# Optimization experiments

Measured on AMD Instinct MI355X. Metric: run time of the kernel, lower is better.

The kernel has to match this reference:

```python
import jax, jax.numpy as jnp
import numpy as np

B, L, DM, DIN, N, R, K, H = 4, 2048, 1024, 2048, 16, 64, 4, 1024
EPS = 1e-5


def setup_inputs() -> dict:
    key = jax.random.key(0)
    ks = jax.random.split(key, 12)
    nrm = lambda k, shp, s=0.02: jax.random.normal(k, shp, jnp.float32) * s
    return dict(
        hidden_states=jax.random.normal(ks[0], (B, L, DM), jnp.float32),
        residual=jax.random.normal(ks[1], (B, L, DM), jnp.float32),
        norm_w=jnp.ones((DM,), jnp.float32),
        in_proj_w=nrm(ks[2], (2 * DIN, DM)),
        conv_w=nrm(ks[3], (DIN, K), 0.2),
        conv_b=jnp.zeros((DIN,), jnp.float32),
        x_proj_w=nrm(ks[4], (R + 2 * N, DIN)),
        dt_proj_w=nrm(ks[5], (DIN, R), 0.1),
        dt_proj_b=jnp.log(jnp.expm1(jnp.full((DIN,), 0.01, jnp.float32))),
        A_log=jnp.log(jnp.tile(jnp.arange(1, N + 1, dtype=jnp.float32), (DIN, 1))),
        D=jnp.ones((DIN,), jnp.float32),
        out_proj_w=nrm(ks[6], (DM, DIN)),
        norm2_w=jnp.ones((DM,), jnp.float32),
        fc1_w=nrm(ks[7], (2 * H, DM)),
        fc2_w=nrm(ks[8], (DM, H)),
    )


def _rmsnorm(x, w):
    return x * jax.lax.rsqrt(jnp.mean(x * x, axis=-1, keepdims=True) + EPS) * w


def _mixer(h, in_proj_w, conv_w, conv_b, x_proj_w, dt_proj_w, dt_proj_b,
           A_log, D, out_proj_w):
    # in_proj -> x, z : (B, L, DIN) each
    xz = jnp.einsum('bld,ed->ble', h, in_proj_w)
    x, z = jnp.split(xz, 2, axis=-1)
    # depthwise causal conv along L
    xc = x.transpose(0, 2, 1)  # (B, DIN, L)
    xc = jax.lax.conv_general_dilated(
        xc, conv_w[:, None, :], window_strides=(1,), padding=[(K - 1, 0)],
        feature_group_count=DIN)
    xc = xc + conv_b[None, :, None]
    x = jax.nn.silu(xc).transpose(0, 2, 1)  # (B, L, DIN)
    # x_proj -> dt_low, B, C
    dbl = jnp.einsum('bld,ed->ble', x, x_proj_w)
    dt_low, Bm, Cm = jnp.split(dbl, [R, R + N], axis=-1)
    dt = jax.nn.softplus(jnp.einsum('blr,dr->bld', dt_low, dt_proj_w) + dt_proj_b)
    A = -jnp.exp(A_log)  # (DIN, N)

    def step(hc, inp):
        dt_t, B_t, C_t, x_t = inp  # (B,DIN),(B,N),(B,N),(B,DIN)
        hc = jnp.exp(dt_t[..., None] * A) * hc + (dt_t * x_t)[..., None] * B_t[:, None, :]
        return hc, jnp.einsum('bdn,bn->bd', hc, C_t)

    h0 = jnp.zeros((B, DIN, N), x.dtype)
    _, ys = jax.lax.scan(step, h0, (dt.transpose(1, 0, 2), Bm.transpose(1, 0, 2),
                                    Cm.transpose(1, 0, 2), x.transpose(1, 0, 2)))
    y = ys.transpose(1, 0, 2) + x * D  # skip term D*u
    y = y * jax.nn.silu(z)
    return jnp.einsum('bld,ed->ble', y, out_proj_w)


def reference(hidden_states, residual, norm_w, in_proj_w, conv_w, conv_b,
              x_proj_w, dt_proj_w, dt_proj_b, A_log, D, out_proj_w,
              norm2_w, fc1_w, fc2_w):
    # pre-norm residual path (fused_add_norm=False, residual_in_fp32=True)
    res = hidden_states + residual
    hn = _rmsnorm(res, norm_w)
    mix = _mixer(hn, in_proj_w, conv_w, conv_b, x_proj_w, dt_proj_w,
                 dt_proj_b, A_log, D, out_proj_w)
    # NOTE: faithful to source: residual is overwritten by norm2(mix+res),
    # while mlp is applied to the raw mixer output.
    res2 = _rmsnorm(mix + res, norm2_w)
    fc = jnp.einsum('bld,hd->blh', mix, fc1_w)
    y, gate = jnp.split(fc, 2, axis=-1)
    out = jnp.einsum('blh,dh->bld', y * jax.nn.silu(gate), fc2_w)
    return (out, res2)
```

## Files before the change

kernel.cpp:

```cpp
#include <hip/hip_runtime.h>
#include <hip/hip_bf16.h>

#define B_   4
#define L_   2048
#define DM_  1024
#define DIN_ 2048
#define NS_  16
#define R_   64
#define KC_  4
#define H_   1024
#define BL_  (B_ * L_)

typedef __attribute__((ext_vector_type(4))) float f32x4;
typedef __attribute__((ext_vector_type(8))) short bf16x8;
typedef __attribute__((ext_vector_type(8))) unsigned short u16x8;

#if __has_builtin(__builtin_amdgcn_exp2f)
#define EXP2(x) __builtin_amdgcn_exp2f(x)
#else
#define EXP2(x) exp2f(x)
#endif
#define LOG2E 1.44269504088896f

__device__ __forceinline__ float b2f(unsigned short u) {
    union { unsigned int i; float f; } v; v.i = ((unsigned int)u) << 16; return v.f;
}
__device__ __forceinline__ unsigned short f2b(float f) {
    union { float f; unsigned int i; } v; v.f = f;
    unsigned int r = v.i + 0x7fffu + ((v.i >> 16) & 1u);
    return (unsigned short)(r >> 16);
}
__device__ __forceinline__ float sigmoidf_(float x) { return 1.f / (1.f + __expf(-x)); }
__device__ __forceinline__ float softplusf_(float x) { return (x > 20.f) ? x : log1pf(__expf(x)); }

__device__ __forceinline__ void gload16(const unsigned short* g, unsigned short* l) {
    __builtin_amdgcn_global_load_lds(
        (__attribute__((address_space(1))) void*)(g),
        (__attribute__((address_space(3))) void*)(l), 16, 0, 0);
}

__global__ void k_cvt4(const float* __restrict__ in, unsigned short* __restrict__ out, int n4) {
    int i = blockIdx.x * blockDim.x + threadIdx.x;
    if (i < n4) {
        float4 v = ((const float4*)in)[i];
        ((ushort4*)out)[i] = make_ushort4(f2b(v.x), f2b(v.y), f2b(v.z), f2b(v.w));
    }
}
__global__ void k_fill04(unsigned short* __restrict__ out, int n4) {
    int i = blockIdx.x * blockDim.x + threadIdx.x;
    if (i < n4) ((ushort4*)out)[i] = make_ushort4(0, 0, 0, 0);
}

__global__ __launch_bounds__(256)
void k_reduceX(const float* __restrict__ part, unsigned short* __restrict__ dblB,
               float* __restrict__ dblF) {
    int i = blockIdx.x * 256 + threadIdx.x;
    if (i >= BL_ * 96) return;
    int r = i / 96, n = i - r * 96;
    const float* p = part + (size_t)r * 2048;
    float s = p[n] + p[128 + n] + p[256 + n] + p[384 + n];
    dblB[(size_t)r * 96 + n] = f2b(s);
    if (n >= 64) dblF[(size_t)r * 32 + n - 64] = s;
}

__global__ __launch_bounds__(256)
void k_add_rmsnorm(const float* __restrict__ a, const float* __restrict__ b,
                   const float* __restrict__ w,
                   float* __restrict__ resOut, unsigned short* __restrict__ hnOut) {
    int row = blockIdx.x, tid = threadIdx.x;
    const float4* ap = (const float4*)(a + (size_t)row * DM_);
    const float4* bp = (const float4*)(b + (size_t)row * DM_);
    float4 va = ap[tid], vb = bp[tid];
    float4 s = make_float4(va.x + vb.x, va.y + vb.y, va.z + vb.z, va.w + vb.w);
    ((float4*)(resOut + (size_t)row * DM_))[tid] = s;
    float ss = s.x * s.x + s.y * s.y + s.z * s.z + s.w * s.w;
    #pragma unroll
    for (int m = 32; m >= 1; m >>= 1) ss += __shfl_xor(ss, m);
    __shared__ float red[4];
    if ((tid & 63) == 0) red[tid >> 6] = ss;
    __syncthreads();
    float tot = red[0] + red[1] + red[2] + red[3];
    float sc = rsqrtf(tot / (float)DM_ + 1e-5f);
    float4 vw = ((const float4*)w)[tid];
    unsigned short* hp = hnOut + (size_t)row * DM_ + tid * 4;
    *(ushort4*)hp = make_ushort4(f2b(s.x * sc * vw.x), f2b(s.y * sc * vw.y),
                                 f2b(s.z * sc * vw.z), f2b(s.w * sc * vw.w));
}

__global__ __launch_bounds__(256)
void k_add_rmsnorm2(const float* __restrict__ mix, const float* __restrict__ res,
                    const float* __restrict__ w,
                    float* __restrict__ res2Out, unsigned short* __restrict__ mixB) {
    int row = blockIdx.x, tid = threadIdx.x;
    const float4* mp = (const float4*)(mix + (size_t)row * DM_);
    const float4* rp = (const float4*)(res + (size_t)row * DM_);
    float4 vm = mp[tid], vr = rp[tid];
    float4 s = make_float4(vm.x + vr.x, vm.y + vr.y, vm.z + vr.z, vm.w + vr.w);
    unsigned short* mb = mixB + (size_t)row * DM_ + tid * 4;
    *(ushort4*)mb = make_ushort4(f2b(vm.x), f2b(vm.y), f2b(vm.z), f2b(vm.w));
    float ss = s.x * s.x + s.y * s.y + s.z * s.z + s.w * s.w;
    #pragma unroll
    for (int m = 32; m >= 1; m >>= 1) ss += __shfl_xor(ss, m);
    __shared__ float red[4];
    if ((tid & 63) == 0) red[tid >> 6] = ss;
    __syncthreads();
    float tot = red[0] + red[1] + red[2] + red[3];
    float sc = rsqrtf(tot / (float)DM_ + 1e-5f);
    float4 vw = ((const float4*)w)[tid];
    float4 o = make_float4(s.x * sc * vw.x, s.y * sc * vw.y, s.z * sc * vw.z, s.w * sc * vw.w);
    ((float4*)(res2Out + (size_t)row * DM_))[tid] = o;
}

__global__ __launch_bounds__(256)
void k_conv_silu(const unsigned short* __restrict__ xz,
                 const float* __restrict__ cw, const float* __restrict__ cb,
                 unsigned short* __restrict__ xc) {
    const int tid = threadIdx.x;
    const int d0 = tid * 8;
    const int b  = blockIdx.x >> 8;
    const int t0 = (blockIdx.x & 255) * 8;
    const unsigned short* xbase = xz + (size_t)b * L_ * (2 * DIN_) + d0;
    unsigned short* obase = xc + (size_t)b * L_ * DIN_ + d0;

    float4 w[8];
    float bias[8];
    #pragma unroll
    for (int j = 0; j < 8; j++) {
        w[j] = ((const float4*)cw)[d0 + j];
        bias[j] = cb[d0 + j];
    }
    u16x8 zero = (u16x8){0, 0, 0, 0, 0, 0, 0, 0};
    u16x8 r0 = zero, r1 = zero, r2 = zero, r3;
    if (t0 >= 3) {
        r0 = *(const u16x8*)(xbase + (size_t)(t0 - 3) * (2 * DIN_));
        r1 = *(const u16x8*)(xbase + (size_t)(t0 - 2) * (2 * DIN_));
        r2 = *(const u16x8*)(xbase + (size_t)(t0 - 1) * (2 * DIN_));
    }
    #pragma unroll
    for (int tt = 0; tt < 8; tt++) {
        int t = t0 + tt;
        r3 = *(const u16x8*)(xbase + (size_t)t * (2 * DIN_));
        u16x8 out;
        #pragma unroll
        for (int j = 0; j < 8; j++) {
            float acc = bias[j] + w[j].x * b2f(r0[j]) + w[j].y * b2f(r1[j])
                                + w[j].z * b2f(r2[j]) + w[j].w * b2f(r3[j]);
            out[j] = f2b(acc * sigmoidf_(acc));
        }
        *(u16x8*)(obase + (size_t)t * DIN_) = out;
        r0 = r1; r1 = r2; r2 = r3;
    }
}

__global__ __launch_bounds__(256)
void k_gate(const unsigned short* __restrict__ fc, unsigned short* __restrict__ g) {
    int i = blockIdx.x * 256 + threadIdx.x;
    int row = i >> 7;
    int h8 = (i & 127) * 8;
    u16x8 y8 = *(const u16x8*)(fc + (size_t)row * (2 * H_) + h8);
    u16x8 g8 = *(const u16x8*)(fc + (size_t)row * (2 * H_) + H_ + h8);
    u16x8 o;
    #pragma unroll
    for (int j = 0; j < 8; j++) {
        float y = b2f(y8[j]), gt = b2f(g8[j]);
        o[j] = f2b(y * gt * sigmoidf_(gt));
    }
    *(u16x8*)(g + (size_t)row * H_ + h8) = o;
}

template <int CHLT>
__global__ __launch_bounds__(256)
void k_scan_p1(const unsigned short* __restrict__ dty, const unsigned short* __restrict__ xc,
               const float* __restrict__ dblF, const float* __restrict__ A_log,
               unsigned short* __restrict__ Q, unsigned short* __restrict__ sumdt, int cch) {
    const int tid = threadIdx.x;
    const int d = (blockIdx.x & 7) * 256 + tid;
    const int b = blockIdx.x >> 3;
    const int c = blockIdx.y;
    const int t0 = c * CHLT;

    float a[NS_], h[NS_];
    #pragma unroll
    for (int n = 0; n < NS_; n++) { a[n] = -__expf(A_log[d * NS_ + n]) * LOG2E; h[n] = 0.f; }
    float sd = 0.f;

    const unsigned short* dp  = dty + (size_t)b * L_ * DIN_ + d;
    const unsigned short* xp  = xc  + (size_t)b * L_ * DIN_ + d;
    const float* bcp = dblF + (size_t)(b * L_ + t0) * 32;

    #pragma unroll 2
    for (int t = 0; t < CHLT; t++) {
        int tg = t0 + t;
        float dtv = b2f(dp[(size_t)tg * DIN_]);
        float xv  = b2f(xp[(size_t)tg * DIN_]);
        sd += dtv;
        float bx = dtv * xv;
        const float* bc = bcp + t * 32;
        #pragma unroll
        for (int n = 0; n < NS_; n++)
            h[n] = EXP2(dtv * a[n]) * h[n] + bx * bc[n];
    }
    unsigned short* q = Q + ((size_t)(b * cch + c) * DIN_ + d) * NS_;
    u16x8 qa, qb;
    #pragma unroll
    for (int j = 0; j < 8; j++) { qa[j] = f2b(h[j]); qb[j] = f2b(h[8 + j]); }
    *(u16x8*)q = qa;
    *(u16x8*)(q + 8) = qb;
    sumdt[(size_t)(b * cch + c) * DIN_ + d] = f2b(sd);
}

__global__ __launch_bounds__(256)
void k_scan_comb(unsigned short* __restrict__ Q, const unsigned short* __restrict__ sumdt,
                 const float* __restrict__ A_log, int cch) {
    int i = blockIdx.x * 256 + threadIdx.x;
    int n = i & 15;
    int d = (i >> 4) & (DIN_ - 1);
    int b = i >> 15;
    float a = -__expf(A_log[d * NS_ + n]) * LOG2E;
    float h = 0.f;
    for (int c = 0; c < cch; c++) {
        size_t base = ((size_t)(b * cch + c) * DIN_ + d);
        float q  = b2f(Q[base * NS_ + n]);
        float sd = b2f(sumdt[base]);
        if (c > 0) Q[((size_t)(b * cch + c - 1) * DIN_ + d) * NS_ + n] = f2b(h);
        h = EXP2(a * sd) * h + q;
    }
}

template <int CHLT>
__global__ __launch_bounds__(256)
void k_scan_p3(unsigned short* __restrict__ dty, const unsigned short* __restrict__ xc,
               const float* __restrict__ dblF, const float* __restrict__ A_log,
               const float* __restrict__ Dp, const unsigned short* __restrict__ xz,
               const unsigned short* __restrict__ Qh, int cch) {
    const int tid = threadIdx.x;
    const int d = (blockIdx.x & 7) * 256 + tid;
    const int b = blockIdx.x >> 3;
    const int c = blockIdx.y;
    const int t0 = c * CHLT;

    float a[NS_], h[NS_];
    #pragma unroll
    for (int n = 0; n < NS_; n++) a[n] = -__expf(A_log[d * NS_ + n]) * LOG2E;
    if (c == 0) {
        #pragma unroll
        for (int n = 0; n < NS_; n++) h[n] = 0.f;
    } else {
        const unsigned short* qh = Qh + ((size_t)(b * cch + c - 1) * DIN_ + d) * NS_;
        u16x8 v0 = *(const u16x8*)qh;
        u16x8 v1 = *(const u16x8*)(qh + 8);
        #pragma unroll
        for (int j = 0; j < 8; j++) { h[j] = b2f(v0[j]); h[8 + j] = b2f(v1[j]); }
    }
    float Dd = Dp[d];

    unsigned short* dp = dty + (size_t)b * L_ * DIN_ + d;
    const unsigned short* xp  = xc + (size_t)b * L_ * DIN_ + d;
    const unsigned short* zp  = xz + (size_t)b * L_ * (2 * DIN_) + DIN_ + d;
    const float* bcp = dblF + (size_t)(b * L_ + t0) * 32;

    #pragma unroll 2
    for (int t = 0; t < CHLT; t++) {
        int tg = t0 + t;
        float dtv = b2f(dp[(size_t)tg * DIN_]);
        float xv  = b2f(xp[(size_t)tg * DIN_]);
        float bx = dtv * xv;
        const float* bc = bcp + t * 32;
        float y = 0.f;
        #pragma unroll
        for (int n = 0; n < NS_; n++) {
            h[n] = EXP2(dtv * a[n]) * h[n] + bx * bc[n];
            y += h[n] * bc[16 + n];
        }
        y += xv * Dd;
        float zv = b2f(zp[(size_t)tg * (2 * DIN_)]);
        dp[(size_t)tg * DIN_] = f2b(y * zv * sigmoidf_(zv));
    }
}

template <int EPI, int SPLITK = 0>
__global__ __launch_bounds__(256)
void k_gemm(const unsigned short* __restrict__ A, int lda,
            const unsigned short* __restrict__ Bw, int ldb,
            void* __restrict__ outp, int ldc, const float* __restrict__ bias,
            int M, int N, int Kd, int Nstore) {
    if constexpr (SPLITK) {
        const int z = blockIdx.z;
        A += (size_t)z * 512;
        Bw += (size_t)z * 512;
        outp = (void*)((float*)outp + z * 128);
    }
    __shared__ unsigned short As[128 * 32];
    __shared__ unsigned short Bs[128 * 32];
    const int tid = threadIdx.x;
    const int lane = tid & 63;
    const int w = tid >> 6;
    const int wr = w >> 1, wc = w & 1;
    const int bm = blockIdx.y * 128, bn = blockIdx.x * 128;

    const int e0 = tid * 8;
    const int r0 = e0 >> 5;
    const int c0 = e0 & 31;
    const int r1 = r0 + 64;

    f32x4 acc[4][4];
    #pragma unroll
    for (int i = 0; i < 4; i++)
        #pragma unroll
        for (int j = 0; j < 4; j++) acc[i][j] = (f32x4){0.f, 0.f, 0.f, 0.f};

    const int fr = lane & 15, ko = (lane >> 4) * 8;

    for (int k0 = 0; k0 < Kd; k0 += 32) {
        gload16(A  + (size_t)(bm + r0) * lda + k0 + c0, &As[e0]);
        gload16(A  + (size_t)(bm + r1) * lda + k0 + c0, &As[e0 + 2048]);
        gload16(Bw + (size_t)(bn + r0) * ldb + k0 + c0, &Bs[e0]);
        gload16(Bw + (size_t)(bn + r1) * ldb + k0 + c0, &Bs[e0 + 2048]);
        __syncthreads();
        bf16x8 af[4], bv[4];
        #pragma unroll
        for (int i = 0; i < 4; i++)
            af[i] = *(const bf16x8*)&As[(wr * 64 + i * 16 + fr) * 32 + ko];
        #pragma unroll
        for (int j = 0; j < 4; j++)
            bv[j] = *(const bf16x8*)&Bs[(wc * 64 + j * 16 + fr) * 32 + ko];
        #pragma unroll
        for (int i = 0; i < 4; i++)
            #pragma unroll
            for (int j = 0; j < 4; j++)
                acc[i][j] = __builtin_amdgcn_mfma_f32_16x16x32_bf16(af[i], bv[j], acc[i][j], 0, 0, 0);
        __syncthreads();
    }

    const int rr = (lane >> 4) * 4;
    const int cc = lane & 15;
    #pragma unroll
    for (int i = 0; i < 4; i++) {
        #pragma unroll
        for (int j = 0; j < 4; j++) {
            int col = bn + wc * 64 + j * 16 + cc;
            if (col >= Nstore) continue;
            #pragma unroll
            for (int q = 0; q < 4; q++) {
                int row = bm + wr * 64 + i * 16 + rr + q;
                float v = acc[i][j][q];
                if constexpr (EPI == 2) { v += bias[col]; v = softplusf_(v); }
                if constexpr (EPI == 0)
                    ((float*)outp)[(size_t)row * ldc + col] = v;
                else
                    ((unsigned short*)outp)[(size_t)row * ldc + col] = f2b(v);
            }
        }
    }
}

#define SBAR   __builtin_amdgcn_s_barrier()
#define SCHED0 __builtin_amdgcn_sched_barrier(0)
#define SLOT(r) ((((r) ^ ((r) >> 2)) & 3) << 4)

template <int EPI, int BN>
__global__ __launch_bounds__(512, 2)
void k_gemm256(const unsigned short* __restrict__ Aptr, int lda,
               const unsigned short* __restrict__ Bptr, int ldb,
               void* __restrict__ outp, int ldc, int Kd) {
    extern __shared__ unsigned short lds[];
    constexpr int WN = BN / 64;
    constexpr int MF = (BN == 256) ? 8 : 4;
    constexpr int BSL = BN * 32;
    constexpr int BBASE = 32768;
    const int tid  = threadIdx.x;
    const int lane = tid & 63;
    const int wid  = tid >> 6;
    const int wr = wid / WN, wc = wid % WN;

    const int gdx = (int)gridDim.x;
    const int nwg = gdx * (int)gridDim.y;
    const int orig = (int)blockIdx.y * gdx + (int)blockIdx.x;
    const int cpx = nwg >> 3;
    const int swz = (orig & 7) * cpx + (orig >> 3);
    const int bm = (swz / gdx) * 256, bn = (swz % gdx) * BN;

    const int fr = lane & 15, sk = lane >> 4;

    f32x4 acc[MF][4];
    #pragma unroll
    for (int i = 0; i < MF; i++)
        #pragma unroll
        for (int j = 0; j < 4; j++) acc[i][j] = (f32x4){0.f, 0.f, 0.f, 0.f};

    const int NT = Kd >> 6;

    const int o0 = tid * 16, o1 = (512 + tid) * 16;
    const int sr0 = o0 >> 6, sr1 = o1 >> 6;
    const int sc0 = (o0 & 63) ^ SLOT(sr0);
    const int sc1 = (o1 & 63) ^ SLOT(sr1);
    const unsigned short* Ag0 = Aptr + (size_t)(bm + sr0) * lda + (sc0 >> 1);
    const unsigned short* Ag1 = Aptr + (size_t)(bm + sr1) * lda + (sc1 >> 1);
    const unsigned short* Bg0 = Bptr + (size_t)(bn + sr0) * ldb + (sc0 >> 1);
    const unsigned short* Bg1 = Bptr + (size_t)(bn + sr1) * ldb + (sc1 >> 1);
    unsigned short* LA0 = lds + (o0 >> 1);
    unsigned short* LA1 = lds + (o1 >> 1);
    unsigned short* LB0 = lds + BBASE + (o0 >> 1);
    unsigned short* LB1 = lds + BBASE + (o1 >> 1);

    auto stageA = [&](int buf, int ks, int kt) {
        int s = (buf * 2 + ks) * 8192;
        gload16(Ag0 + kt * 64 + ks * 32, LA0 + s);
        gload16(Ag1 + kt * 64 + ks * 32, LA1 + s);
    };
    auto stageB = [&](int buf, int ks, int kt) {
        int s = (buf * 2 + ks) * BSL;
        gload16(Bg0 + kt * 64 + ks * 32, LB0 + s);
        if constexpr (BN == 256) gload16(Bg1 + kt * 64 + ks * 32, LB1 + s);
    };

    const int rsw  = (sk * 16) ^ SLOT(fr);
    const int aoff = (wr * (MF * 16) + fr) * 32 + (rsw >> 1);
    const int boff = (wc * 64 + fr) * 32 + (rsw >> 1);

#define DSREAD_B(buf, ks) { _Pragma("unroll") for (int n = 0; n < 4; n++) \
    bv[n] = *(const bf16x8*)&lds[BBASE + ((buf)*2+(ks))*BSL + boff + n*512]; }
#define DSREAD_A4(buf, ks, mh) { _Pragma("unroll") for (int m = 0; m < 4; m++) \
    af[m] = *(const bf16x8*)&lds[((buf)*2+(ks))*8192 + aoff + ((mh)*4+m)*512]; }
#define MFMA16(mh) { __builtin_amdgcn_s_setprio(1); \
    _Pragma("unroll") for (int m = 0; m < 4; m++) \
      _Pragma("unroll") for (int n = 0; n < 4; n++) \
        acc[(mh)*4+m][n] = __builtin_amdgcn_mfma_f32_16x16x32_bf16(af[m], bv[n], acc[(mh)*4+m][n], 0, 0, 0); \
    __builtin_amdgcn_s_setprio(0); }

    if constexpr (BN == 256) {
        stageA(0, 0, 0); stageB(0, 0, 0); stageA(0, 1, 0); stageB(0, 1, 0);
        SCHED0;
        asm volatile("s_waitcnt vmcnt(4)" ::: "memory");
        SBAR;

        int buf = 0;
        for (int kt = 0; kt < NT - 1; ++kt) {
            bf16x8 af[4], bv[4];
            DSREAD_B(buf, 0); DSREAD_A4(buf, 0, 0);
            stageA(buf ^ 1, 0, kt + 1);
            SCHED0; SBAR;
            MFMA16(0);
            SCHED0; SBAR;
            DSREAD_A4(buf, 0, 1);
            stageB(buf ^ 1, 0, kt + 1);
            SCHED0; SBAR;
            MFMA16(1);
            SCHED0;
            asm volatile("s_waitcnt vmcnt(4)" ::: "memory");
            SBAR;
            DSREAD_B(buf, 1); DSREAD_A4(buf, 1, 0);
            stageA(buf ^ 1, 1, kt + 1);
            SCHED0; SBAR;
            MFMA16(0);
            SCHED0; SBAR;
            DSREAD_A4(buf, 1, 1);
            stageB(buf ^ 1, 1, kt + 1);
            SCHED0; SBAR;
            MFMA16(1);
            SCHED0;
            asm volatile("s_waitcnt vmcnt(4)" ::: "memory");
            SBAR;
            buf ^= 1;
        }
        {
            bf16x8 af[4], bv[4];
            DSREAD_B(buf, 0); DSREAD_A4(buf, 0, 0);
            SCHED0; SBAR;
            MFMA16(0);
            SCHED0; SBAR;
            DSREAD_A4(buf, 0, 1);
            SCHED0; SBAR;
            MFMA16(1);
            SCHED0;
            asm volatile("s_waitcnt vmcnt(0)" ::: "memory");
            SBAR;
            DSREAD_B(buf, 1); DSREAD_A4(buf, 1, 0);
            SCHED0; SBAR;
            MFMA16(0);
            SCHED0; SBAR;
            DSREAD_A4(buf, 1, 1);
            SCHED0; SBAR;
            MFMA16(1);
        }
    } else {
        stageA(0, 0, 0); stageB(0, 0, 0); stageA(0, 1, 0); stageB(0, 1, 0);
        SCHED0;
        asm volatile("s_waitcnt vmcnt(3)" ::: "memory");
        SBAR;

        int buf = 0;
        for (int kt = 0; kt < NT - 1; ++kt) {
            bf16x8 af[4], bv[4];
            DSREAD_B(buf, 0); DSREAD_A4(buf, 0, 0);
            stageA(buf ^ 1, 0, kt + 1); stageB(buf ^ 1, 0, kt + 1);
            SCHED0; SBAR;
            MFMA16(0);
            SCHED0;
            asm volatile("s_waitcnt vmcnt(3)" ::: "memory");
            SBAR;
            DSREAD_B(buf, 1); DSREAD_A4(buf, 1, 0);
            stageA(buf ^ 1, 1, kt + 1); stageB(buf ^ 1, 1, kt + 1);
            SCHED0; SBAR;
            MFMA16(0);
            SCHED0;
            asm volatile("s_waitcnt vmcnt(3)" ::: "memory");
            SBAR;
            buf ^= 1;
        }
        {
            bf16x8 af[4], bv[4];
            DSREAD_B(buf, 0); DSREAD_A4(buf, 0, 0);
            SCHED0; SBAR;
            MFMA16(0);
            SCHED0;
            asm volatile("s_waitcnt vmcnt(0)" ::: "memory");
            SBAR;
            DSREAD_B(buf, 1); DSREAD_A4(buf, 1, 0);
            SCHED0; SBAR;
            MFMA16(0);
        }
    }
#undef DSREAD_B
#undef DSREAD_A4
#undef MFMA16

    const int rr = sk * 4;
    const int cc = fr;
    #pragma unroll
    for (int mf = 0; mf < MF; mf++) {
        #pragma unroll
        for (int nf = 0; nf < 4; nf++) {
            int col = bn + wc * 64 + nf * 16 + cc;
            #pragma unroll
            for (int q = 0; q < 4; q++) {
                int row = bm + wr * (MF * 16) + mf * 16 + rr + q;
                float v = acc[mf][nf][q];
                if constexpr (EPI == 0)
                    ((float*)outp)[(size_t)row * ldc + col] = v;
                else
                    ((unsigned short*)outp)[(size_t)row * ldc + col] = f2b(v);
            }
        }
    }
}

extern "C" void kernel_launch(void* const* d_in, const int* in_sizes, int n_in,
                              void* d_out, int out_size, void* d_ws, size_t ws_size,
                              hipStream_t stream) {
    const float* hs        = (const float*)d_in[0];
    const float* resi      = (const float*)d_in[1];
    const float* norm_w    = (const float*)d_in[2];
    const float* in_proj_w = (const float*)d_in[3];
    const float* conv_w    = (const float*)d_in[4];
    const float* conv_b    = (const float*)d_in[5];
    const float* x_proj_w  = (const float*)d_in[6];
    const float* dt_proj_w = (const float*)d_in[7];
    const float* dt_proj_b = (const float*)d_in[8];
    const float* A_log     = (const float*)d_in[9];
    const float* Dp        = (const float*)d_in[10];
    const float* out_proj_w= (const float*)d_in[11];
    const float* norm2_w   = (const float*)d_in[12];
    const float* fc1_w     = (const float*)d_in[13];
    const float* fc2_w     = (const float*)d_in[14];

    static bool attrDone = false;
    if (!attrDone) {
        hipFuncSetAttribute(reinterpret_cast<const void*>(k_gemm256<0, 256>),
                            hipFuncAttributeMaxDynamicSharedMemorySize, 131072);
        hipFuncSetAttribute(reinterpret_cast<const void*>(k_gemm256<1, 256>),
                            hipFuncAttributeMaxDynamicSharedMemorySize, 131072);
        hipFuncSetAttribute(reinterpret_cast<const void*>(k_gemm256<0, 128>),
                            hipFuncAttributeMaxDynamicSharedMemorySize, 98304);
        attrDone = true;
    }

    char* ws = (char*)d_ws;
    size_t off = 0;
    auto alloc = [&](size_t bytes) {
        void* p = ws + off;
        off = (off + bytes + 255) & ~(size_t)255;
        return p;
    };

    unsigned short* xzB  = (unsigned short*)alloc((size_t)BL_ * 2 * DIN_ * 2);
    unsigned short* fcB  = xzB;
    unsigned short* gB   = xzB + (size_t)BL_ * 2 * H_;
    unsigned short* mixB = gB  + (size_t)BL_ * H_;
    void* S_xc = alloc((size_t)BL_ * DIN_ * 2);
    unsigned short* hnB    = (unsigned short*)S_xc;
    unsigned short* xconvB = (unsigned short*)S_xc;
    float*          mixF   = (float*)S_xc;
    unsigned short* dblB = (unsigned short*)alloc((size_t)BL_ * 96 * 2);
    unsigned short* inprojB  = (unsigned short*)alloc((size_t)2 * DIN_ * DM_ * 2);
    unsigned short* xprojB   = (unsigned short*)alloc((size_t)128 * DIN_ * 2);
    unsigned short* dtprojB  = (unsigned short*)alloc((size_t)DIN_ * R_ * 2);
    unsigned short* outprojB = (unsigned short*)alloc((size_t)DM_ * DIN_ * 2);
    unsigned short* fc1B     = (unsigned short*)alloc((size_t)2 * H_ * DM_ * 2);
    unsigned short* fc2B     = (unsigned short*)alloc((size_t)DM_ * H_ * 2);
    float*          dblF     = (float*)alloc((size_t)BL_ * 32 * 4);

    unsigned short *scanQ, *scanSd;
    int cch;
    {
        size_t needQ  = (size_t)B_ * 64 * DIN_ * NS_ * 2;
        size_t needSd = (size_t)B_ * 64 * DIN_ * 2;
        if (ws_size >= off + needQ + needSd + 512) {
            scanQ  = (unsigned short*)alloc(needQ);
            scanSd = (unsigned short*)alloc(needSd);
            cch = 64;
        } else {
            scanQ  = inprojB;
            scanSd = xprojB;
            cch = 32;
        }
    }

    float* outMain = (float*)d_out;
    float* outRes2 = (float*)d_out + (size_t)BL_ * DM_;
    float*          resF = outMain;
    unsigned short* dtyB = (unsigned short*)outRes2;

    {
        int n;
        n = 2 * DIN_ * DM_ / 4; k_cvt4<<<(n + 255) / 256, 256, 0, stream>>>(in_proj_w, inprojB, n);
        n = 96 * DIN_ / 4;      k_cvt4<<<(n + 255) / 256, 256, 0, stream>>>(x_proj_w, xprojB, n);
        n = 32 * DIN_ / 4;      k_fill04<<<(n + 255) / 256, 256, 0, stream>>>(xprojB + 96 * DIN_, n);
        n = DIN_ * R_ / 4;      k_cvt4<<<(n + 255) / 256, 256, 0, stream>>>(dt_proj_w, dtprojB, n);
        n = DM_ * DIN_ / 4;     k_cvt4<<<(n + 255) / 256, 256, 0, stream>>>(out_proj_w, outprojB, n);
        n = 2 * H_ * DM_ / 4;   k_cvt4<<<(n + 255) / 256, 256, 0, stream>>>(fc1_w, fc1B, n);
        n = DM_ * H_ / 4;       k_cvt4<<<(n + 255) / 256, 256, 0, stream>>>(fc2_w, fc2B, n);
    }

    k_add_rmsnorm<<<BL_, 256, 0, stream>>>(hs, resi, norm_w, resF, hnB);

    k_gemm256<1, 256><<<dim3(2 * DIN_ / 256, BL_ / 256), 512, 131072, stream>>>(
        hnB, DM_, inprojB, DM_, (void*)xzB, 2 * DIN_, DM_);

    k_conv_silu<<<B_ * 256, 256, 0, stream>>>(xzB, conv_w, conv_b, xconvB);

    k_gemm<0, 1><<<dim3(1, BL_ / 128, 4), 256, 0, stream>>>(
        xconvB, DIN_, xprojB, DIN_, (void*)(float*)xzB, 2048, nullptr, BL_, 128, 512, 128);

    k_reduceX<<<(BL_ * 96 + 255) / 256, 256, 0, stream>>>((const float*)xzB, dblB, dblF);

    k_gemm<2><<<dim3(DIN_ / 128, BL_ / 128), 256, 0, stream>>>(
        dblB, 96, dtprojB, R_, (void*)dtyB, DIN_, dt_proj_b, BL_, DIN_, R_, DIN_);

    if (cch == 64) {
        k_scan_p1<32><<<dim3(B_ * (DIN_ / 256), 64), 256, 0, stream>>>(
            dtyB, xconvB, dblF, A_log, scanQ, scanSd, 64);
        k_scan_comb<<<(B_ * DIN_ * NS_) / 256, 256, 0, stream>>>(scanQ, scanSd, A_log, 64);
        k_scan_p3<32><<<dim3(B_ * (DIN_ / 256), 64), 256, 0, stream>>>(
            dtyB, xconvB, dblF, A_log, Dp, xzB, scanQ, 64);
    } else {
        k_scan_p1<64><<<dim3(B_ * (DIN_ / 256), 32), 256, 0, stream>>>(
            dtyB, xconvB, dblF, A_log, scanQ, scanSd, 32);
        k_scan_comb<<<(B_ * DIN_ * NS_) / 256, 256, 0, stream>>>(scanQ, scanSd, A_log, 32);
        k_scan_p3<64><<<dim3(B_ * (DIN_ / 256), 32), 256, 0, stream>>>(
            dtyB, xconvB, dblF, A_log, Dp, xzB, scanQ, 32);
    }

    k_gemm256<0, 128><<<dim3(DM_ / 128, BL_ / 256), 512, 98304, stream>>>(
        dtyB, DIN_, outprojB, DIN_, (void*)mixF, DM_, DIN_);

    k_add_rmsnorm2<<<BL_, 256, 0, stream>>>(mixF, resF, norm2_w, outRes2, mixB);

    k_gemm256<1, 256><<<dim3(2 * H_ / 256, BL_ / 256), 512, 131072, stream>>>(
        mixB, DM_, fc1B, DM_, (void*)fcB, 2 * H_, DM_);

    k_gate<<<(BL_ * H_ / 8) / 256, 256, 0, stream>>>(fcB, gB);

    k_gemm256<0, 128><<<dim3(DM_ / 128, BL_ / 256), 512, 98304, stream>>>(
        gB, H_, fc2B, H_, (void*)outMain, DM_, H_);
}
```

Baseline: 475.7 us.

## Fuse SwiGLU gate into fc1 GEMM epilogue via interleaved fc1 weights

fc1 weight rows are reordered during bf16 conversion so that each 32-row block holds 16 value rows followed by 16 gate rows. The fc1 GEMM epilogue can then compute y*silu(gate) in registers and write only the gated H-wide bf16 result. This removes the separate k_gate kernel and the write and re-read of the 2H-wide fc intermediate. The weight conversions are also batched into one launch to cut launch overhead. The epilogue writes become strided half-width stores, and the interleaved layout ties correctness to the MFMA fragment mapping.

```diff
diff --git a/kernel.cpp b/kernel.cpp
--- a/kernel.cpp
+++ b/kernel.cpp
@@ -39,13 +39,39 @@
         (__attribute__((address_space(3))) void*)(l), 16, 0, 0);
 }
 
-__global__ void k_cvt4(const float* __restrict__ in, unsigned short* __restrict__ out, int n4) {
-    int i = blockIdx.x * blockDim.x + threadIdx.x;
-    if (i < n4) {
-        float4 v = ((const float4*)in)[i];
-        ((ushort4*)out)[i] = make_ushort4(f2b(v.x), f2b(v.y), f2b(v.z), f2b(v.w));
-    }
-}
+__global__ __launch_bounds__(256)
+void k_cvt5(const float* __restrict__ s0, unsigned short* __restrict__ d0, int n0,
+            const float* __restrict__ s1, unsigned short* __restrict__ d1, int n1,
+            const float* __restrict__ s2, unsigned short* __restrict__ d2, int n2,
+            const float* __restrict__ s3, unsigned short* __restrict__ d3, int n3,
+            const float* __restrict__ s4, unsigned short* __restrict__ d4, int n4) {
+    int j = blockIdx.x * 256 + threadIdx.x;
+    const float* s; unsigned short* d;
+    if (j < n0) { s = s0; d = d0; }
+    else { j -= n0;
+    if (j < n1) { s = s1; d = d1; }
+    else { j -= n1;
+    if (j < n2) { s = s2; d = d2; }
+    else { j -= n2;
+    if (j < n3) { s = s3; d = d3; }
+    else { j -= n3;
+    if (j >= n4) return; s = s4; d = d4; } } } }
+    float4 v = ((const float4*)s)[j];
+    ((ushort4*)d)[j] = make_ushort4(f2b(v.x), f2b(v.y), f2b(v.z), f2b(v.w));
+}
+
+__global__ __launch_bounds__(256)
+void k_cvt_fc1(const float* __restrict__ w, unsigned short* __restrict__ out) {
+    int i = blockIdx.x * 256 + threadIdx.x;
+    if (i >= 2 * H_ * DM_ / 4) return;
+    int col4 = i & (DM_ / 4 - 1);
+    int nrow = i / (DM_ / 4);
+    int blk = nrow >> 5, s = nrow & 31;
+    int srow = (s < 16) ? (blk * 16 + s) : (H_ + blk * 16 + (s - 16));
+    float4 v = ((const float4*)(w + (size_t)srow * DM_))[col4];
+    ((ushort4*)out)[i] = make_ushort4(f2b(v.x), f2b(v.y), f2b(v.z), f2b(v.w));
+}
+
 __global__ void k_fill04(unsigned short* __restrict__ out, int n4) {
     int i = blockIdx.x * blockDim.x + threadIdx.x;
     if (i < n4) ((ushort4*)out)[i] = make_ushort4(0, 0, 0, 0);
@@ -150,22 +176,6 @@
         *(u16x8*)(obase + (size_t)t * DIN_) = out;
         r0 = r1; r1 = r2; r2 = r3;
     }
-}
-
-__global__ __launch_bounds__(256)
-void k_gate(const unsigned short* __restrict__ fc, unsigned short* __restrict__ g) {
-    int i = blockIdx.x * 256 + threadIdx.x;
-    int row = i >> 7;
-    int h8 = (i & 127) * 8;
-    u16x8 y8 = *(const u16x8*)(fc + (size_t)row * (2 * H_) + h8);
-    u16x8 g8 = *(const u16x8*)(fc + (size_t)row * (2 * H_) + H_ + h8);
-    u16x8 o;
-    #pragma unroll
-    for (int j = 0; j < 8; j++) {
-        float y = b2f(y8[j]), gt = b2f(g8[j]);
-        o[j] = f2b(y * gt * sigmoidf_(gt));
-    }
-    *(u16x8*)(g + (size_t)row * H_ + h8) = o;
 }
 
 template <int CHLT>
@@ -527,19 +537,36 @@
 
     const int rr = sk * 4;
     const int cc = fr;
-    #pragma unroll
-    for (int mf = 0; mf < MF; mf++) {
-        #pragma unroll
-        for (int nf = 0; nf < 4; nf++) {
-            int col = bn + wc * 64 + nf * 16 + cc;
+    if constexpr (EPI == 3) {
+        #pragma unroll
+        for (int mf = 0; mf < MF; mf++) {
             #pragma unroll
-            for (int q = 0; q < 4; q++) {
-                int row = bm + wr * (MF * 16) + mf * 16 + rr + q;
-                float v = acc[mf][nf][q];
-                if constexpr (EPI == 0)
-                    ((float*)outp)[(size_t)row * ldc + col] = v;
-                else
-                    ((unsigned short*)outp)[(size_t)row * ldc + col] = f2b(v);
+            for (int nf = 0; nf < 4; nf += 2) {
+                int hcol = ((bn + wc * 64) >> 1) + (nf >> 1) * 16 + cc;
+                #pragma unroll
+                for (int q = 0; q < 4; q++) {
+                    int row = bm + wr * (MF * 16) + mf * 16 + rr + q;
+                    float y = acc[mf][nf][q], gt = acc[mf][nf + 1][q];
+                    ((unsigned short*)outp)[(size_t)row * ldc + hcol] =
+                        f2b(y * gt * sigmoidf_(gt));
+                }
+            }
+        }
+    } else {
+        #pragma unroll
+        for (int mf = 0; mf < MF; mf++) {
+            #pragma unroll
+            for (int nf = 0; nf < 4; nf++) {
+                int col = bn + wc * 64 + nf * 16 + cc;
+                #pragma unroll
+                for (int q = 0; q < 4; q++) {
+                    int row = bm + wr * (MF * 16) + mf * 16 + rr + q;
+                    float v = acc[mf][nf][q];
+                    if constexpr (EPI == 0)
+                        ((float*)outp)[(size_t)row * ldc + col] = v;
+                    else
+                        ((unsigned short*)outp)[(size_t)row * ldc + col] = f2b(v);
+                }
             }
         }
     }
@@ -570,6 +597,8 @@
                             hipFuncAttributeMaxDynamicSharedMemorySize, 131072);
         hipFuncSetAttribute(reinterpret_cast<const void*>(k_gemm256<1, 256>),
                             hipFuncAttributeMaxDynamicSharedMemorySize, 131072);
+        hipFuncSetAttribute(reinterpret_cast<const void*>(k_gemm256<3, 256>),
+                            hipFuncAttributeMaxDynamicSharedMemorySize, 131072);
         hipFuncSetAttribute(reinterpret_cast<const void*>(k_gemm256<0, 128>),
                             hipFuncAttributeMaxDynamicSharedMemorySize, 98304);
         attrDone = true;
@@ -584,9 +613,8 @@
     };
 
     unsigned short* xzB  = (unsigned short*)alloc((size_t)BL_ * 2 * DIN_ * 2);
-    unsigned short* fcB  = xzB;
-    unsigned short* gB   = xzB + (size_t)BL_ * 2 * H_;
-    unsigned short* mixB = gB  + (size_t)BL_ * H_;
+    unsigned short* gB   = xzB;
+    unsigned short* mixB = xzB + (size_t)BL_ * H_;
     void* S_xc = alloc((size_t)BL_ * DIN_ * 2);
     unsigned short* hnB    = (unsigned short*)S_xc;
     unsigned short* xconvB = (unsigned short*)S_xc;
@@ -622,14 +650,19 @@
     unsigned short* dtyB = (unsigned short*)outRes2;
 
     {
-        int n;
-        n = 2 * DIN_ * DM_ / 4; k_cvt4<<<(n + 255) / 256, 256, 0, stream>>>(in_proj_w, inprojB, n);
-        n = 96 * DIN_ / 4;      k_cvt4<<<(n + 255) / 256, 256, 0, stream>>>(x_proj_w, xprojB, n);
-        n = 32 * DIN_ / 4;      k_fill04<<<(n + 255) / 256, 256, 0, stream>>>(xprojB + 96 * DIN_, n);
-        n = DIN_ * R_ / 4;      k_cvt4<<<(n + 255) / 256, 256, 0, stream>>>(dt_proj_w, dtprojB, n);
-        n = DM_ * DIN_ / 4;     k_cvt4<<<(n + 255) / 256, 256, 0, stream>>>(out_proj_w, outprojB, n);
-        n = 2 * H_ * DM_ / 4;   k_cvt4<<<(n + 255) / 256, 256, 0, stream>>>(fc1_w, fc1B, n);
-        n = DM_ * H_ / 4;       k_cvt4<<<(n + 255) / 256, 256, 0, stream>>>(fc2_w, fc2B, n);
+        int n0 = 2 * DIN_ * DM_ / 4;
+        int n1 = 96 * DIN_ / 4;
+        int n2 = DIN_ * R_ / 4;
+        int n3 = DM_ * DIN_ / 4;
+        int n4 = DM_ * H_ / 4;
+        int tot = n0 + n1 + n2 + n3 + n4;
+        k_cvt5<<<(tot + 255) / 256, 256, 0, stream>>>(
+            in_proj_w, inprojB, n0, x_proj_w, xprojB, n1, dt_proj_w, dtprojB, n2,
+            out_proj_w, outprojB, n3, fc2_w, fc2B, n4);
+        int nf1 = 2 * H_ * DM_ / 4;
+        k_cvt_fc1<<<(nf1 + 255) / 256, 256, 0, stream>>>(fc1_w, fc1B);
+        int np = 32 * DIN_ / 4;
+        k_fill04<<<(np + 255) / 256, 256, 0, stream>>>(xprojB + 96 * DIN_, np);
     }
 
     k_add_rmsnorm<<<BL_, 256, 0, stream>>>(hs, resi, norm_w, resF, hnB);
@@ -666,10 +699,8 @@
 
     k_add_rmsnorm2<<<BL_, 256, 0, stream>>>(mixF, resF, norm2_w, outRes2, mixB);
 
-    k_gemm256<1, 256><<<dim3(2 * H_ / 256, BL_ / 256), 512, 131072, stream>>>(
-        mixB, DM_, fc1B, DM_, (void*)fcB, 2 * H_, DM_);
-
-    k_gate<<<(BL_ * H_ / 8) / 256, 256, 0, stream>>>(fcB, gB);
+    k_gemm256<3, 256><<<dim3(2 * H_ / 256, BL_ / 256), 512, 131072, stream>>>(
+        mixB, DM_, fc1B, DM_, (void*)gB, H_, DM_);
 
     k_gemm256<0, 128><<<dim3(DM_ / 128, BL_ / 256), 512, 98304, stream>>>(
         gB, H_, fc2B, H_, (void*)outMain, DM_, H_);
```

Result: faster. 462.7 us (-2.7%).
